# Performance work log

Measured on AMD Instinct MI355X. Metric: run time of the kernel, lower is better.

Reference implementation:

```python
import jax, jax.numpy as jnp
import numpy as np

GROUP = 64
DIM = 4096
N_HEADS = 32
N_KV = 8
HEAD_DIM = DIM // N_HEADS  # 128
N_REP = N_HEADS // N_KV    # 4
B = 1
S = 2048
THETA = 1e6


def _pack_q40(rng, out_f, in_f):
    """Random int4 weights packed Q4_0 style (two nibbles per int8) + per-group scales."""
    q = rng.integers(-7, 8, size=(out_f * in_f,)).reshape(-1, 2, GROUP)
    packed = ((q[:, 0] << 4) | (q[:, 1] & 15)).astype(np.int8)  # [out*in/group/2, group]
    scale = (np.abs(rng.standard_normal((out_f * in_f // GROUP, 1))) * 0.01 + 1e-3).astype(np.float32)
    return jnp.asarray(packed), jnp.asarray(scale)


def dequantize_q40(w, scale, shape):
    """Faithful port of torch dequantize_q40: arithmetic shifts sign-extend nibbles."""
    msb = jnp.right_shift(w, 4)                          # high nibble, sign-extended
    lsb = jnp.right_shift(jnp.left_shift(w, 4), 4)       # low nibble, sign-extended
    grp = jnp.concatenate([msb, lsb], axis=1).reshape(-1, GROUP)  # hstack then view(-1, group)
    return (grp.astype(scale.dtype) * scale).reshape(shape)


def setup_inputs() -> dict:
    rng = np.random.default_rng(0)
    wq, sq = _pack_q40(rng, N_HEADS * HEAD_DIM, DIM)
    wk, sk = _pack_q40(rng, N_KV * HEAD_DIM, DIM)
    wv, sv = _pack_q40(rng, N_KV * HEAD_DIM, DIM)
    wo, so = _pack_q40(rng, DIM, N_HEADS * HEAD_DIM)
    x = jnp.asarray(rng.standard_normal((B, S, DIM)), jnp.float32)
    inv_freq = 1.0 / (THETA ** (np.arange(0, HEAD_DIM, 2, dtype=np.float64) / HEAD_DIM))
    ang = np.outer(np.arange(S, dtype=np.float64), inv_freq)  # [S, HEAD_DIM/2]
    cos = jnp.asarray(np.cos(ang), jnp.float32)
    sin = jnp.asarray(np.sin(ang), jnp.float32)
    causal = np.triu(np.ones((S, S), dtype=bool), k=1)
    mask = jnp.asarray(np.where(causal, -1e9, 0.0), jnp.float32)
    return dict(x=x, wq=wq, sq=sq, wk=wk, sk=sk, wv=wv, sv=sv, wo=wo, so=so,
                cos=cos, sin=sin, mask=mask)


def _rotate_half(t):
    h = t.shape[-1] // 2
    return jnp.concatenate([-t[..., h:], t[..., :h]], axis=-1)


def reference(x, wq, sq, wk, sk, wv, sv, wo, so, cos, sin, mask):
    # Dequant-then-matmul QKV projections (weights stored as [out, in])
    Wq = dequantize_q40(wq, sq, (N_HEADS * HEAD_DIM, DIM))
    Wk = dequantize_q40(wk, sk, (N_KV * HEAD_DIM, DIM))
    Wv = dequantize_q40(wv, sv, (N_KV * HEAD_DIM, DIM))
    Wo = dequantize_q40(wo, so, (DIM, N_HEADS * HEAD_DIM))

    xq = (x @ Wq.T).reshape(B, S, N_HEADS, HEAD_DIM)
    xk = (x @ Wk.T).reshape(B, S, N_KV, HEAD_DIM)
    xv = (x @ Wv.T).reshape(B, S, N_KV, HEAD_DIM)

    # RoPE (rotate-half convention): cos/sin are [S, HEAD_DIM/2] -> cat to [S, HEAD_DIM]
    cosf = jnp.concatenate([cos, cos], axis=-1)[:, None, :]  # [S, 1, HEAD_DIM]
    sinf = jnp.concatenate([sin, sin], axis=-1)[:, None, :]
    xq = xq * cosf + _rotate_half(xq) * sinf
    xk = xk * cosf + _rotate_half(xk) * sinf

    # start_pos == 0 prefill: keys/values are the freshly projected xk/xv
    # GQA: repeat_interleave over the kv-head dim
    keys = jnp.repeat(xk, N_REP, axis=2)    # [B, S, N_HEADS, HEAD_DIM]
    values = jnp.repeat(xv, N_REP, axis=2)

    scores = jnp.einsum('bqhd,bkhd->bhqk', xq, keys) / np.float32(np.sqrt(HEAD_DIM))
    scores = scores + mask  # additive causal mask broadcast over [B, H]
    attn = jax.nn.softmax(scores, axis=-1)
    out = jnp.einsum('bhqk,bkhd->bqhd', attn, values).reshape(B, S, N_HEADS * HEAD_DIM)
    return out @ Wo.T
```

## Files before the change

kernel.cpp:

```cpp
#include <hip/hip_runtime.h>
#include <stdint.h>

#define DIMX 4096
#define NH   32
#define NKV  8
#define HD   128
#define SEQ  2048
#define QKVD 6144

typedef _Float16 h16;
typedef __attribute__((ext_vector_type(8))) _Float16 h16x8;
typedef __attribute__((ext_vector_type(4))) _Float16 h16x4;
typedef __attribute__((ext_vector_type(4))) float   f32x4;

__device__ __forceinline__ void gload_lds16(const void* g, void* l) {
  __builtin_amdgcn_global_load_lds(
      (const __attribute__((address_space(1))) void*)g,
      (__attribute__((address_space(3))) void*)l, 16, 0, 0);
}

template <int CTRL>
__device__ __forceinline__ float dpp_mv(float x) {
  int y = __builtin_amdgcn_mov_dpp(__builtin_bit_cast(int, x), CTRL, 0xF, 0xF, true);
  return __builtin_bit_cast(float, y);
}
__device__ __forceinline__ float red16_max(float x) {
  x = fmaxf(x, dpp_mv<0xB1>(x));
  x = fmaxf(x, dpp_mv<0x1B>(x));
  x = fmaxf(x, dpp_mv<0x141>(x));
  x = fmaxf(x, dpp_mv<0x140>(x));
  return x;
}
__device__ __forceinline__ float red16_sum(float x) {
  x += dpp_mv<0xB1>(x);
  x += dpp_mv<0x1B>(x);
  x += dpp_mv<0x141>(x);
  x += dpp_mv<0x140>(x);
  return x;
}

__device__ __forceinline__ void dq_unit(const void* __restrict__ w, const float* __restrict__ sc,
                                        h16* __restrict__ out, int u, int flag) {
  uint32_t b4;
  if (flag) {
    const int4 t = *(const int4*)((const int*)w + 4 * u);
    b4 = (uint32_t)(t.x & 0xFF) | ((uint32_t)(t.y & 0xFF) << 8) |
         ((uint32_t)(t.z & 0xFF) << 16) | ((uint32_t)(t.w & 0xFF) << 24);
  } else {
    b4 = ((const uint32_t*)w)[u];
  }
  int r = u >> 4;
  int p = (u & 15) * 4;
  float shi = sc[2 * r], slo = sc[2 * r + 1];
  h16x4 hi, lo;
#pragma unroll
  for (int j = 0; j < 4; ++j) {
    int by = (int)((b4 >> (8 * j)) & 0xFF);
    int hn = (by << 24) >> 28;
    int ln = (by << 28) >> 28;
    hi[j] = (h16)((float)hn * shi);
    lo[j] = (h16)((float)ln * slo);
  }
  *(h16x4*)(out + (r << 7) + p)      = hi;
  *(h16x4*)(out + (r << 7) + 64 + p) = lo;
}

#define U_WQ 2097152
#define U_WK 524288
#define U_WV 524288
#define U_WO 2097152

__global__ __launch_bounds__(256) void prep_all(
    const void* __restrict__ wq, const float* __restrict__ sq,
    const void* __restrict__ wk, const float* __restrict__ sk,
    const void* __restrict__ wv, const float* __restrict__ sv,
    const void* __restrict__ wo, const float* __restrict__ so,
    const float4* __restrict__ x,
    h16* __restrict__ Wqkv, h16* __restrict__ Wo, h16x4* __restrict__ xb) {
  __shared__ int sfl;
  if (threadIdx.x == 0) {
    int ok = 1;
    const int* wi = (const int*)wq;
    for (int i = 0; i < 64; ++i) {
      int v = wi[i];
      if (v < -128 || v > 127) ok = 0;
    }
    sfl = ok;
  }
  __syncthreads();
  const int fl = sfl;
  int u = blockIdx.x * 256 + threadIdx.x;
  if (u < U_WQ) { dq_unit(wq, sq, Wqkv, u, fl); return; }
  u -= U_WQ;
  if (u < U_WK) { dq_unit(wk, sk, Wqkv + 16777216, u, fl); return; }
  u -= U_WK;
  if (u < U_WV) { dq_unit(wv, sv, Wqkv + 20971520, u, fl); return; }
  u -= U_WV;
  if (u < U_WO) { dq_unit(wo, so, Wo, u, fl); return; }
  u -= U_WO;
  {
    float4 v = x[u];
    h16x4 o;
    o.x = (h16)v.x; o.y = (h16)v.y; o.z = (h16)v.z; o.w = (h16)v.w;
    xb[u] = o;
  }
}

template <typename OutT>
__global__ __launch_bounds__(256) void gemm_bt(
    const h16* __restrict__ A, const h16* __restrict__ B,
    OutT* __restrict__ C, int M, int N, int K) {
  __shared__ __attribute__((aligned(16))) h16 As[128 * 64];
  __shared__ __attribute__((aligned(16))) h16 Bs[128 * 64];
  const int tid  = threadIdx.x;
  const int wv   = tid >> 6, lane = tid & 63;
  const int wr   = wv >> 1,  wc   = wv & 1;
  const int quad = lane >> 4, l15 = lane & 15;
  const int m0 = blockIdx.y * 128, n0 = blockIdx.x * 128;

  f32x4 acc[4][4];
#pragma unroll
  for (int i = 0; i < 4; ++i)
#pragma unroll
    for (int j = 0; j < 4; ++j) acc[i][j] = (f32x4){0.f, 0.f, 0.f, 0.f};

  const h16* Ab = A + (size_t)m0 * K;
  const h16* Bb = B + (size_t)n0 * K;

  for (int k0 = 0; k0 < K; k0 += 64) {
    __syncthreads();
#pragma unroll
    for (int i = 0; i < 4; ++i) {
      int c = i * 256 + tid;
      int row = c >> 3, cs = c & 7;
      int g = cs ^ (row & 7);
      gload_lds16(Ab + (size_t)row * K + k0 + g * 8, (char*)As + c * 16);
      gload_lds16(Bb + (size_t)row * K + k0 + g * 8, (char*)Bs + c * 16);
    }
    __syncthreads();

#pragma unroll
    for (int ks = 0; ks < 2; ++ks) {
      h16x8 af[4], bfr[4];
#pragma unroll
      for (int mt = 0; mt < 4; ++mt) {
        int row = wr * 64 + mt * 16 + l15;
        af[mt] = *(const h16x8*)&As[row * 64 + (((ks * 4 + quad) ^ (row & 7)) * 8)];
      }
#pragma unroll
      for (int nt = 0; nt < 4; ++nt) {
        int row = wc * 64 + nt * 16 + l15;
        bfr[nt] = *(const h16x8*)&Bs[row * 64 + (((ks * 4 + quad) ^ (row & 7)) * 8)];
      }
#pragma unroll
      for (int mt = 0; mt < 4; ++mt)
#pragma unroll
        for (int nt = 0; nt < 4; ++nt)
          acc[mt][nt] = __builtin_amdgcn_mfma_f32_16x16x32_f16(af[mt], bfr[nt], acc[mt][nt], 0, 0, 0);
    }
  }
#pragma unroll
  for (int mt = 0; mt < 4; ++mt)
#pragma unroll
    for (int nt = 0; nt < 4; ++nt)
#pragma unroll
      for (int r = 0; r < 4; ++r) {
        int row = m0 + wr * 64 + mt * 16 + quad * 4 + r;
        int col = n0 + wc * 64 + nt * 16 + l15;
        C[(size_t)row * N + col] = (OutT)acc[mt][nt][r];
      }
}

__global__ __launch_bounds__(256) void rope_vtrans(
    h16* __restrict__ qkv, const float* __restrict__ cosb, const float* __restrict__ sinb,
    h16* __restrict__ vt) {
  __shared__ h16 T[64 * 66];
  int b = blockIdx.x;
  if (b < 5120) {
    int idx = b * 256 + threadIdx.x;
    int d4 = (idx & 15) * 4;
    int t  = idx >> 4;
    int hh = t % 40;
    int s  = t / 40;
    int base = (hh < 32) ? (s * QKVD + hh * 128)
                         : (s * QKVD + 4096 + (hh - 32) * 128);
    h16x4 a = *(const h16x4*)(qkv + base + d4);
    h16x4 bb = *(const h16x4*)(qkv + base + 64 + d4);
    float4 c  = *(const float4*)(cosb + s * 64 + d4);
    float4 sn = *(const float4*)(sinb + s * 64 + d4);
    h16x4 oa, ob;
    oa.x = (h16)((float)a.x * c.x - (float)bb.x * sn.x);
    oa.y = (h16)((float)a.y * c.y - (float)bb.y * sn.y);
    oa.z = (h16)((float)a.z * c.z - (float)bb.z * sn.z);
    oa.w = (h16)((float)a.w * c.w - (float)bb.w * sn.w);
    ob.x = (h16)((float)bb.x * c.x + (float)a.x * sn.x);
    ob.y = (h16)((float)bb.y * c.y + (float)a.y * sn.y);
    ob.z = (h16)((float)bb.z * c.z + (float)a.z * sn.z);
    ob.w = (h16)((float)bb.w * c.w + (float)a.w * sn.w);
    *(h16x4*)(qkv + base + d4)      = oa;
    *(h16x4*)(qkv + base + 64 + d4) = ob;
  } else {
    int i = b - 5120;
    int kv = i >> 6;
    int rem = i & 63;
    int d0 = (rem >> 5) * 64, s0 = (rem & 31) * 64;
    const int t = threadIdx.x;
#pragma unroll
    for (int i2 = 0; i2 < 4; ++i2) {
      int s = i2 * 16 + (t >> 4), dd = (t & 15) * 4;
      h16x4 v = *(const h16x4*)(qkv + (size_t)(s0 + s) * QKVD + 5120 + kv * 128 + d0 + dd);
      *(h16x4*)&T[s * 66 + dd] = v;
    }
    __syncthreads();
#pragma unroll
    for (int i2 = 0; i2 < 4; ++i2) {
      int dr = i2 * 16 + (t >> 4), s4 = (t & 15) * 4;
      h16x4 o;
#pragma unroll
      for (int j = 0; j < 4; ++j) o[j] = T[(s4 + j) * 66 + dr];
      *(h16x4*)(vt + (size_t)kv * HD * SEQ + (size_t)(d0 + dr) * SEQ + s0 + s4) = o;
    }
  }
}

__global__ __launch_bounds__(256, 2) void flash_attn(
    const h16* __restrict__ qkv, const h16* __restrict__ vt, h16* __restrict__ o_out) {
  __shared__ __attribute__((aligned(16))) h16 Ks[64 * 128];
  __shared__ __attribute__((aligned(16))) h16 Vts[128 * 64];
  __shared__ __attribute__((aligned(16))) h16 Ps[4][32 * 72];

  const int tid  = threadIdx.x;
  const int w    = tid >> 6, lane = tid & 63;
  const int quad = lane >> 4, l15 = lane & 15;
  const int h    = blockIdx.x;
  const int y    = blockIdx.y;
  const int qt   = (y < 8) ? (15 - y) : (y - 8);
  const int kv   = h >> 2;
  const int rowq = qt * 128 + w * 32;
  const h16* vtg = vt + (size_t)kv * HD * SEQ;

  h16x8 qf[2][4];
#pragma unroll
  for (int mt = 0; mt < 2; ++mt) {
    const h16* qrow = qkv + (size_t)(rowq + mt * 16 + l15) * QKVD + h * 128;
#pragma unroll
    for (int ks = 0; ks < 4; ++ks)
      qf[mt][ks] = *(const h16x8*)(qrow + ks * 32 + quad * 8);
  }

  f32x4 o[2][8];
#pragma unroll
  for (int mt = 0; mt < 2; ++mt)
#pragma unroll
    for (int i = 0; i < 8; ++i) o[mt][i] = (f32x4){0.f, 0.f, 0.f, 0.f};
  float mrow[2][4], lrow[2][4];
#pragma unroll
  for (int mt = 0; mt < 2; ++mt)
#pragma unroll
    for (int r = 0; r < 4; ++r) { mrow[mt][r] = -3e30f; lrow[mt][r] = 0.f; }
  h16* Psw = Ps[w];

  const int nkt = 2 * qt + 2;
  for (int kt = 0; kt < nkt; ++kt) {
    const int k0 = kt * 64;
    __syncthreads();
#pragma unroll
    for (int i = 0; i < 4; ++i) {
      int c = i * 256 + tid;
      int key = c >> 4, d8s = c & 15;
      gload_lds16(qkv + (size_t)(k0 + key) * QKVD + 4096 + kv * 128 + (d8s ^ (key & 15)) * 8,
                  (char*)Ks + c * 16);
    }
#pragma unroll
    for (int i = 0; i < 4; ++i) {
      int c = i * 256 + tid;
      int d = c >> 3, p = c & 7;
      gload_lds16(vtg + (size_t)d * SEQ + k0 + (p ^ (d & 7)) * 8,
                  (char*)Vts + c * 16);
    }
    __syncthreads();

    if (k0 <= rowq + 31) {
      const float sscale = 0.08838834764831845f;
      float alpha[2][4];
      f32x4 s2[2][4];
#pragma unroll
      for (int nt = 0; nt < 4; ++nt) {
        int key = nt * 16 + l15;
        f32x4 a0 = (f32x4){0.f, 0.f, 0.f, 0.f};
        f32x4 a1 = (f32x4){0.f, 0.f, 0.f, 0.f};
#pragma unroll
        for (int ks = 0; ks < 4; ++ks) {
          int d8 = ks * 4 + quad;
          h16x8 kf = *(const h16x8*)&Ks[key * 128 + ((d8 ^ (key & 15)) * 8)];
          a0 = __builtin_amdgcn_mfma_f32_16x16x32_f16(qf[0][ks], kf, a0, 0, 0, 0);
          a1 = __builtin_amdgcn_mfma_f32_16x16x32_f16(qf[1][ks], kf, a1, 0, 0, 0);
        }
        s2[0][nt] = a0;
        s2[1][nt] = a1;
      }
#pragma unroll
      for (int mt = 0; mt < 2; ++mt) {
#pragma unroll
        for (int r = 0; r < 4; ++r) {
          int rowg = rowq + mt * 16 + quad * 4 + r;
          float pv[4];
          float tm = -3e30f;
#pragma unroll
          for (int nt = 0; nt < 4; ++nt) {
            float v = s2[mt][nt][r] * sscale;
            if (k0 + nt * 16 + l15 > rowg) v = -3e30f;
            pv[nt] = v;
            tm = fmaxf(tm, v);
          }
          tm = red16_max(tm);
          float mnew = fmaxf(mrow[mt][r], tm);
          float a = __expf(mrow[mt][r] - mnew);
          mrow[mt][r] = mnew;
          alpha[mt][r] = a;
          float ps = 0.f;
#pragma unroll
          for (int nt = 0; nt < 4; ++nt) {
            float e = __expf(pv[nt] - mnew);
            ps += e;
            Psw[(mt * 16 + quad * 4 + r) * 72 + nt * 16 + l15] = (h16)e;
          }
          ps = red16_sum(ps);
          lrow[mt][r] = lrow[mt][r] * a + ps;
        }
      }
#pragma unroll
      for (int mt = 0; mt < 2; ++mt)
#pragma unroll
        for (int on = 0; on < 8; ++on) {
          o[mt][on][0] *= alpha[mt][0]; o[mt][on][1] *= alpha[mt][1];
          o[mt][on][2] *= alpha[mt][2]; o[mt][on][3] *= alpha[mt][3];
        }
      asm volatile("s_waitcnt lgkmcnt(0)" ::: "memory");
#pragma unroll
      for (int ks = 0; ks < 2; ++ks) {
        h16x8 pf0 = *(const h16x8*)&Psw[(0  + l15) * 72 + ks * 32 + quad * 8];
        h16x8 pf1 = *(const h16x8*)&Psw[(16 + l15) * 72 + ks * 32 + quad * 8];
        int k8 = ks * 4 + quad;
#pragma unroll
        for (int on = 0; on < 8; ++on) {
          int d = on * 16 + l15;
          h16x8 vf = *(const h16x8*)&Vts[d * 64 + ((k8 ^ (d & 7)) * 8)];
          o[0][on] = __builtin_amdgcn_mfma_f32_16x16x32_f16(pf0, vf, o[0][on], 0, 0, 0);
          o[1][on] = __builtin_amdgcn_mfma_f32_16x16x32_f16(pf1, vf, o[1][on], 0, 0, 0);
        }
      }
    }
  }
#pragma unroll
  for (int mt = 0; mt < 2; ++mt) {
    float linv[4];
#pragma unroll
    for (int r = 0; r < 4; ++r) linv[r] = 1.0f / lrow[mt][r];
#pragma unroll
    for (int on = 0; on < 8; ++on)
#pragma unroll
      for (int r = 0; r < 4; ++r) {
        int row = rowq + mt * 16 + quad * 4 + r;
        int col = h * 128 + on * 16 + l15;
        o_out[(size_t)row * DIMX + col] = (h16)(o[mt][on][r] * linv[r]);
      }
  }
}

extern "C" void kernel_launch(void* const* d_in, const int* in_sizes, int n_in,
                              void* d_out, int out_size, void* d_ws, size_t ws_size,
                              hipStream_t stream) {
  const float* x    = (const float*)d_in[0];
  const void*  wq   = d_in[1];
  const float* sq   = (const float*)d_in[2];
  const void*  wk   = d_in[3];
  const float* sk   = (const float*)d_in[4];
  const void*  wv   = d_in[5];
  const float* sv   = (const float*)d_in[6];
  const void*  wo   = d_in[7];
  const float* so   = (const float*)d_in[8];
  const float* cosb = (const float*)d_in[9];
  const float* sinb = (const float*)d_in[10];
  float* out = (float*)d_out;

  char* ws = (char*)d_ws;
  h16* Wqkv = (h16*)ws;
  h16* Wo   = (h16*)(ws + 50331648);
  h16* xb   = (h16*)(ws + 83886080);
  h16* qkv  = (h16*)(ws + 100663296);
  h16* vt   = (h16*)ws;

  prep_all<<<28672, 256, 0, stream>>>(wq, sq, wk, sk, wv, sv, wo, so,
                                      (const float4*)x, Wqkv, Wo, (h16x4*)xb);

  gemm_bt<h16><<<dim3(48, 16), 256, 0, stream>>>(xb, Wqkv, qkv, SEQ, QKVD, DIMX);

  rope_vtrans<<<5632, 256, 0, stream>>>(qkv, cosb, sinb, vt);

  flash_attn<<<dim3(32, 16), 256, 0, stream>>>(qkv, vt, xb);

  gemm_bt<float><<<dim3(32, 16), 256, 0, stream>>>(xb, Wo, out, SEQ, DIMX, DIMX);
}
```

Measured before the change: 482.5 us.

## Fuse RoPE and V transpose into QKV GEMM epilogue; narrow output GEMM tile

```diff
diff --git a/kernel.cpp b/kernel.cpp
--- a/kernel.cpp
+++ b/kernel.cpp
@@ -106,23 +106,31 @@
   }
 }
 
-template <typename OutT>
+template <typename OutT, int NT, int MODE>
 __global__ __launch_bounds__(256) void gemm_bt(
     const h16* __restrict__ A, const h16* __restrict__ B,
-    OutT* __restrict__ C, int M, int N, int K) {
-  __shared__ __attribute__((aligned(16))) h16 As[128 * 64];
-  __shared__ __attribute__((aligned(16))) h16 Bs[128 * 64];
+    OutT* __restrict__ C, int M, int N, int K,
+    const float* __restrict__ cosb, const float* __restrict__ sinb,
+    h16* __restrict__ vt) {
+  constexpr int BN = NT * 32;
+  constexpr int SAB = 128 * 64 + BN * 64;
+  constexpr int SSZ = (MODE == 1 && 128 * 136 > SAB) ? 128 * 136 : SAB;
+  __shared__ __attribute__((aligned(16))) h16 SMEM[SSZ];
+  h16* As = SMEM;
+  h16* Bs = SMEM + 128 * 64;
+  h16* T  = SMEM;
+
   const int tid  = threadIdx.x;
   const int wv   = tid >> 6, lane = tid & 63;
   const int wr   = wv >> 1,  wc   = wv & 1;
   const int quad = lane >> 4, l15 = lane & 15;
-  const int m0 = blockIdx.y * 128, n0 = blockIdx.x * 128;
-
-  f32x4 acc[4][4];
+  const int m0 = blockIdx.y * 128, n0 = blockIdx.x * BN;
+
+  f32x4 acc[4][NT];
 #pragma unroll
   for (int i = 0; i < 4; ++i)
 #pragma unroll
-    for (int j = 0; j < 4; ++j) acc[i][j] = (f32x4){0.f, 0.f, 0.f, 0.f};
+    for (int j = 0; j < NT; ++j) acc[i][j] = (f32x4){0.f, 0.f, 0.f, 0.f};
 
   const h16* Ab = A + (size_t)m0 * K;
   const h16* Bb = B + (size_t)n0 * K;
@@ -132,95 +140,99 @@
 #pragma unroll
     for (int i = 0; i < 4; ++i) {
       int c = i * 256 + tid;
-      int row = c >> 3, cs = c & 7;
-      int g = cs ^ (row & 7);
+      int row = c >> 3, cs = c & 7, g = cs ^ (row & 7);
       gload_lds16(Ab + (size_t)row * K + k0 + g * 8, (char*)As + c * 16);
+    }
+#pragma unroll
+    for (int i = 0; i < NT; ++i) {
+      int c = i * 256 + tid;
+      int row = c >> 3, cs = c & 7, g = cs ^ (row & 7);
       gload_lds16(Bb + (size_t)row * K + k0 + g * 8, (char*)Bs + c * 16);
     }
     __syncthreads();
 
 #pragma unroll
     for (int ks = 0; ks < 2; ++ks) {
-      h16x8 af[4], bfr[4];
+      h16x8 af[4], bfr[NT];
 #pragma unroll
       for (int mt = 0; mt < 4; ++mt) {
         int row = wr * 64 + mt * 16 + l15;
         af[mt] = *(const h16x8*)&As[row * 64 + (((ks * 4 + quad) ^ (row & 7)) * 8)];
       }
 #pragma unroll
-      for (int nt = 0; nt < 4; ++nt) {
-        int row = wc * 64 + nt * 16 + l15;
+      for (int nt = 0; nt < NT; ++nt) {
+        int row = wc * (NT * 16) + nt * 16 + l15;
         bfr[nt] = *(const h16x8*)&Bs[row * 64 + (((ks * 4 + quad) ^ (row & 7)) * 8)];
       }
 #pragma unroll
       for (int mt = 0; mt < 4; ++mt)
 #pragma unroll
-        for (int nt = 0; nt < 4; ++nt)
+        for (int nt = 0; nt < NT; ++nt)
           acc[mt][nt] = __builtin_amdgcn_mfma_f32_16x16x32_f16(af[mt], bfr[nt], acc[mt][nt], 0, 0, 0);
     }
   }
+
+  if (MODE == 1) {
+    if (n0 < 5120) {
+      __syncthreads();
+#pragma unroll
+      for (int mt = 0; mt < 4; ++mt)
+#pragma unroll
+        for (int nt = 0; nt < NT; ++nt)
+#pragma unroll
+          for (int r = 0; r < 4; ++r)
+            T[(wr * 64 + mt * 16 + quad * 4 + r) * 136 + wc * 64 + nt * 16 + l15] =
+                (h16)acc[mt][nt][r];
+      __syncthreads();
+      const int row = tid >> 1, half = tid & 1;
+      const size_t gs = (size_t)(m0 + row);
+#pragma unroll
+      for (int i = 0; i < 8; ++i) {
+        int c0 = half * 32 + i * 4;
+        h16x4 a = *(const h16x4*)&T[row * 136 + c0];
+        h16x4 b = *(const h16x4*)&T[row * 136 + c0 + 64];
+        float4 cc = *(const float4*)(cosb + gs * 64 + c0);
+        float4 ss = *(const float4*)(sinb + gs * 64 + c0);
+        h16x4 oa, ob;
+        oa.x = (h16)((float)a.x * cc.x - (float)b.x * ss.x);
+        oa.y = (h16)((float)a.y * cc.y - (float)b.y * ss.y);
+        oa.z = (h16)((float)a.z * cc.z - (float)b.z * ss.z);
+        oa.w = (h16)((float)a.w * cc.w - (float)b.w * ss.w);
+        ob.x = (h16)((float)b.x * cc.x + (float)a.x * ss.x);
+        ob.y = (h16)((float)b.y * cc.y + (float)a.y * ss.y);
+        ob.z = (h16)((float)b.z * cc.z + (float)a.z * ss.z);
+        ob.w = (h16)((float)b.w * cc.w + (float)a.w * ss.w);
+        *(h16x4*)((h16*)C + gs * N + n0 + c0)      = oa;
+        *(h16x4*)((h16*)C + gs * N + n0 + c0 + 64) = ob;
+      }
+    } else {
+      const int kvh = (n0 - 5120) >> 7;
+      h16* vbase = vt + (size_t)kvh * HD * SEQ;
+#pragma unroll
+      for (int mt = 0; mt < 4; ++mt)
+#pragma unroll
+        for (int nt = 0; nt < NT; ++nt) {
+          int d = wc * 64 + nt * 16 + l15;
+          int s = m0 + wr * 64 + mt * 16 + quad * 4;
+          h16x4 vvv;
+#pragma unroll
+          for (int r = 0; r < 4; ++r) vvv[r] = (h16)acc[mt][nt][r];
+          *(h16x4*)(vbase + (size_t)d * SEQ + s) = vvv;
+        }
+    }
+    return;
+  }
+
 #pragma unroll
   for (int mt = 0; mt < 4; ++mt)
 #pragma unroll
-    for (int nt = 0; nt < 4; ++nt)
+    for (int nt = 0; nt < NT; ++nt)
 #pragma unroll
       for (int r = 0; r < 4; ++r) {
         int row = m0 + wr * 64 + mt * 16 + quad * 4 + r;
-        int col = n0 + wc * 64 + nt * 16 + l15;
+        int col = n0 + wc * (NT * 16) + nt * 16 + l15;
         C[(size_t)row * N + col] = (OutT)acc[mt][nt][r];
       }
-}
-
-__global__ __launch_bounds__(256) void rope_vtrans(
-    h16* __restrict__ qkv, const float* __restrict__ cosb, const float* __restrict__ sinb,
-    h16* __restrict__ vt) {
-  __shared__ h16 T[64 * 66];
-  int b = blockIdx.x;
-  if (b < 5120) {
-    int idx = b * 256 + threadIdx.x;
-    int d4 = (idx & 15) * 4;
-    int t  = idx >> 4;
-    int hh = t % 40;
-    int s  = t / 40;
-    int base = (hh < 32) ? (s * QKVD + hh * 128)
-                         : (s * QKVD + 4096 + (hh - 32) * 128);
-    h16x4 a = *(const h16x4*)(qkv + base + d4);
-    h16x4 bb = *(const h16x4*)(qkv + base + 64 + d4);
-    float4 c  = *(const float4*)(cosb + s * 64 + d4);
-    float4 sn = *(const float4*)(sinb + s * 64 + d4);
-    h16x4 oa, ob;
-    oa.x = (h16)((float)a.x * c.x - (float)bb.x * sn.x);
-    oa.y = (h16)((float)a.y * c.y - (float)bb.y * sn.y);
-    oa.z = (h16)((float)a.z * c.z - (float)bb.z * sn.z);
-    oa.w = (h16)((float)a.w * c.w - (float)bb.w * sn.w);
-    ob.x = (h16)((float)bb.x * c.x + (float)a.x * sn.x);
-    ob.y = (h16)((float)bb.y * c.y + (float)a.y * sn.y);
-    ob.z = (h16)((float)bb.z * c.z + (float)a.z * sn.z);
-    ob.w = (h16)((float)bb.w * c.w + (float)a.w * sn.w);
-    *(h16x4*)(qkv + base + d4)      = oa;
-    *(h16x4*)(qkv + base + 64 + d4) = ob;
-  } else {
-    int i = b - 5120;
-    int kv = i >> 6;
-    int rem = i & 63;
-    int d0 = (rem >> 5) * 64, s0 = (rem & 31) * 64;
-    const int t = threadIdx.x;
-#pragma unroll
-    for (int i2 = 0; i2 < 4; ++i2) {
-      int s = i2 * 16 + (t >> 4), dd = (t & 15) * 4;
-      h16x4 v = *(const h16x4*)(qkv + (size_t)(s0 + s) * QKVD + 5120 + kv * 128 + d0 + dd);
-      *(h16x4*)&T[s * 66 + dd] = v;
-    }
-    __syncthreads();
-#pragma unroll
-    for (int i2 = 0; i2 < 4; ++i2) {
-      int dr = i2 * 16 + (t >> 4), s4 = (t & 15) * 4;
-      h16x4 o;
-#pragma unroll
-      for (int j = 0; j < 4; ++j) o[j] = T[(s4 + j) * 66 + dr];
-      *(h16x4*)(vt + (size_t)kv * HD * SEQ + (size_t)(d0 + dr) * SEQ + s0 + s4) = o;
-    }
-  }
 }
 
 __global__ __launch_bounds__(256, 2) void flash_attn(
@@ -389,16 +401,16 @@
   h16* Wo   = (h16*)(ws + 50331648);
   h16* xb   = (h16*)(ws + 83886080);
   h16* qkv  = (h16*)(ws + 100663296);
-  h16* vt   = (h16*)ws;
+  h16* vt   = (h16*)d_out;
 
   prep_all<<<28672, 256, 0, stream>>>(wq, sq, wk, sk, wv, sv, wo, so,
                                       (const float4*)x, Wqkv, Wo, (h16x4*)xb);
 
-  gemm_bt<h16><<<dim3(48, 16), 256, 0, stream>>>(xb, Wqkv, qkv, SEQ, QKVD, DIMX);
-
-  rope_vtrans<<<5632, 256, 0, stream>>>(qkv, cosb, sinb, vt);
+  gemm_bt<h16, 4, 1><<<dim3(48, 16), 256, 0, stream>>>(
+      xb, Wqkv, qkv, SEQ, QKVD, DIMX, cosb, sinb, vt);
 
   flash_attn<<<dim3(32, 16), 256, 0, stream>>>(qkv, vt, xb);
 
-  gemm_bt<float><<<dim3(32, 16), 256, 0, stream>>>(xb, Wo, out, SEQ, DIMX, DIMX);
-}
+  gemm_bt<float, 2, 0><<<dim3(64, 16), 256, 0, stream>>>(
+      xb, Wo, out, SEQ, DIMX, DIMX, cosb, sinb, vt);
+}
```

Result: faster. 471.7 us (-2.2%).
